# Kernel optimization log

Hardware: AMD Instinct MI355X
Metric: run time of the kernel (lower is better)

Reference implementation:

```python
import jax, jax.numpy as jnp
import numpy as np
import math


def _layernorm(x, g, b, eps=1e-5):
    m = x.mean(-1, keepdims=True)
    v = x.var(-1, keepdims=True)
    return (x - m) / jnp.sqrt(v + eps) * g + b


def _ssd(log_decay, frequency, b_r, b_i, chunk):
    # SSD eigenstate evolution: chunk-local complex decay-mask matmuls + sequential inter-chunk state scan
    B, T, K = b_r.shape
    T_pad = -(-T // chunk) * chunk
    if T_pad > T:
        pad = T_pad - T
        b_r = jnp.pad(b_r, ((0, 0), (0, pad), (0, 0)))
        b_i = jnp.pad(b_i, ((0, 0), (0, pad), (0, 0)))
    n_chunks = T_pad // chunk
    mag = jax.nn.sigmoid(log_decay)                      # (K,)
    pos = jnp.arange(chunk, dtype=b_r.dtype)             # (C,)
    mag_pow = mag[None, :] ** pos[:, None]               # (C,K)
    phases = pos[:, None] * frequency[None, :]           # (C,K)
    kernel_r = mag_pow * jnp.cos(phases)
    kernel_i = mag_pow * jnp.sin(phases)
    diffs = pos[None, :] - pos[:, None]                  # (C,C), faithful to torch: pos.unsqueeze(0)-pos.unsqueeze(1)
    mask = (diffs >= 0).astype(b_r.dtype)[:, :, None]
    idx = jnp.clip(diffs, 0, None).astype(jnp.int32)
    L_r = kernel_r[idx] * mask                           # (C,C,K)
    L_i = kernel_i[idx] * mask
    Br = b_r.reshape(B, n_chunks, chunk, K)
    Bi = b_i.reshape(B, n_chunks, chunk, K)
    # intra-chunk complex contraction
    intra_r = jnp.einsum('ijk,bnjk->bnik', L_r, Br) - jnp.einsum('ijk,bnjk->bnik', L_i, Bi)
    intra_i = jnp.einsum('ijk,bnjk->bnik', L_r, Bi) + jnp.einsum('ijk,bnjk->bnik', L_i, Br)
    prop_r = L_r[:, 0, :]                                # (C,K)
    prop_i = L_i[:, 0, :]

    def step(carry, chunk_in):
        sr, si = carry                                   # (B,K)
        ir, ii = chunk_in                                # (B,C,K)
        corr_r = prop_r[None] * sr[:, None] - prop_i[None] * si[:, None]
        corr_i = prop_r[None] * si[:, None] + prop_i[None] * sr[:, None]
        out_r = ir + corr_r
        out_i = ii + corr_i
        return (out_r[:, -1], out_i[:, -1]), (out_r, out_i)

    init = (jnp.zeros((B, K), b_r.dtype), jnp.zeros((B, K), b_r.dtype))
    _, (o_r, o_i) = jax.lax.scan(step, init, (intra_r.transpose(1, 0, 2, 3), intra_i.transpose(1, 0, 2, 3)))
    c_r = o_r.transpose(1, 0, 2, 3).reshape(B, T_pad, K)[:, :T]
    c_i = o_i.transpose(1, 0, 2, 3).reshape(B, T_pad, K)[:, :T]
    return c_r, c_i


def setup_inputs() -> dict:
    B, T, D, K, H, CONV = 4, 4096, 1024, 64, 4, 4
    Kh = K // H
    mlp = 4 * D
    ks = jax.random.split(jax.random.key(0), 12)

    def n(k, shape, s):
        return (jax.random.normal(k, shape) * s).astype(jnp.float32)

    return {
        'x': n(ks[0], (B, T, D), 1.0),
        'in_proj_w': n(ks[1], (2 * K, D), 1.0 / math.sqrt(D)),
        'conv_w': n(ks[2], (2 * K, 1, CONV), 0.5),
        'conv_b': jnp.zeros((2 * K,), jnp.float32),
        'log_decay': jax.random.uniform(ks[3], (K,), minval=-3.0, maxval=-1.5).astype(jnp.float32),
        'frequency': jnp.linspace(0.0, 2 * math.pi * (1 - 1.0 / K), K).astype(jnp.float32),
        'coupling': (jnp.eye(Kh)[None] + 0.01 * jax.random.normal(ks[4], (H, Kh, Kh)) / math.sqrt(Kh)).astype(jnp.float32),
        'out_proj_w': n(ks[5], (D, 2 * K), 1.0 / math.sqrt(2 * K)),
        'gate_w': n(ks[6], (D, D), 1.0 / math.sqrt(D)),
        'gate_b': jnp.full((D,), -2.0, jnp.float32),
        'mlp_w1': n(ks[7], (mlp, D), 1.0 / math.sqrt(D)),
        'mlp_b1': jnp.zeros((mlp,), jnp.float32),
        'mlp_w2': n(ks[8], (D, mlp), 1.0 / math.sqrt(mlp)),
        'mlp_b2': jnp.zeros((D,), jnp.float32),
        'ln1_g': jnp.ones((D,), jnp.float32), 'ln1_b': jnp.zeros((D,), jnp.float32),
        'ln2_g': jnp.ones((D,), jnp.float32), 'ln2_b': jnp.zeros((D,), jnp.float32),
    }


def reference(x, in_proj_w, conv_w, conv_b, log_decay, frequency, coupling,
              out_proj_w, gate_w, gate_b, mlp_w1, mlp_b1, mlp_w2, mlp_b2,
              ln1_g, ln1_b, ln2_g, ln2_b):
    B, T, D = x.shape
    K2 = in_proj_w.shape[0]
    K = K2 // 2
    CHUNK = 64
    H, Kh = coupling.shape[0], coupling.shape[1]
    residual = x
    xn = _layernorm(x, ln1_g, ln1_b)
    beta = xn @ in_proj_w.T                              # (B,T,2K)
    kconv = conv_w.shape[-1]
    # causal depthwise conv1d (torch pads both sides then truncates to T == left-pad kconv-1)
    bc = jax.lax.conv_general_dilated(
        beta.transpose(0, 2, 1), conv_w, (1,), [(kconv - 1, 0)],
        feature_group_count=K2, dimension_numbers=('NCH', 'OIH', 'NCH'))
    beta = jax.nn.silu((bc + conv_b[None, :, None]).transpose(0, 2, 1))
    beta_r, beta_i = beta[..., :K], beta[..., K:]
    c_r, c_i = _ssd(log_decay, frequency, beta_r, beta_i, CHUNK)
    c_r = jnp.einsum('hjk,bthk->bthj', coupling, c_r.reshape(B, T, H, Kh)).reshape(B, T, K)
    c_i = jnp.einsum('hjk,bthk->bthj', coupling, c_i.reshape(B, T, H, Kh)).reshape(B, T, K)
    eig = jnp.concatenate([c_r, c_i], axis=-1)           # (B,T,2K)
    h = eig @ out_proj_w.T
    gate = jax.nn.sigmoid(xn @ gate_w.T + gate_b)
    x1 = residual + gate * h
    xn2 = _layernorm(x1, ln2_g, ln2_b)
    out = x1 + (jax.nn.silu(xn2 @ mlp_w1.T + mlp_b1) @ mlp_w2.T + mlp_b2)
    return out, eig
```

## Files before the change

kernel.cpp:

```cpp
#include <hip/hip_runtime.h>
#include <hip/hip_bf16.h>


#define FIR_LAG 20

typedef __attribute__((ext_vector_type(8))) short    bf16x8;
typedef __attribute__((ext_vector_type(4))) float    f32x4;
typedef __attribute__((ext_vector_type(4))) unsigned short ushort4_t;

__device__ __forceinline__ unsigned short f2bf(float f) {
    union { __hip_bfloat16 b; unsigned short u; } cv;
    cv.b = __float2bfloat16(f);
    return cv.u;
}
__device__ __forceinline__ float bf2f(unsigned short u) {
    return __uint_as_float((unsigned)u << 16);
}

__device__ __forceinline__ void gload_lds16(const unsigned short* g, unsigned short* l) {
    __builtin_amdgcn_global_load_lds(
        (const __attribute__((address_space(1))) unsigned int*)g,
        (__attribute__((address_space(3))) unsigned int*)l, 16, 0, 0);
}

__global__ __launch_bounds__(256) void cvt5_kernel(
    const float* __restrict__ s0, const float* __restrict__ s1,
    const float* __restrict__ s2, const float* __restrict__ s3,
    const float* __restrict__ s4,
    unsigned short* __restrict__ d0, unsigned short* __restrict__ d1,
    unsigned short* __restrict__ d2, unsigned short* __restrict__ d3,
    unsigned short* __restrict__ d4)
{
    int b = blockIdx.x;
    const float* s; unsigned short* d; int base;
    if      (b < 64)   { s = s0; d = d0; base = b; }
    else if (b < 128)  { s = s1; d = d1; base = b - 64; }
    else if (b < 640)  { s = s2; d = d2; base = b - 128; }
    else if (b < 2688) { s = s3; d = d3; base = b - 640; }
    else               { s = s4; d = d4; base = b - 2688; }
    int i = (base * 256 + threadIdx.x) * 8;
    float4 a = *(const float4*)(s + i);
    float4 c = *(const float4*)(s + i + 4);
    ushort4_t o0 = { f2bf(a.x), f2bf(a.y), f2bf(a.z), f2bf(a.w) };
    ushort4_t o1 = { f2bf(c.x), f2bf(c.y), f2bf(c.z), f2bf(c.w) };
    *(ushort4_t*)(d + i)     = o0;
    *(ushort4_t*)(d + i + 4) = o1;
}

__global__ __launch_bounds__(256) void ln_kernel(
    const float* __restrict__ in, const float* __restrict__ g,
    const float* __restrict__ b, unsigned short* __restrict__ out)
{
    const size_t row = blockIdx.x;
    const int t = threadIdx.x;
    float4 v = ((const float4*)(in + row * 1024))[t];
    float s  = v.x + v.y + v.z + v.w;
    float s2 = v.x*v.x + v.y*v.y + v.z*v.z + v.w*v.w;
    #pragma unroll
    for (int o = 32; o > 0; o >>= 1) {
        s  += __shfl_down(s, o);
        s2 += __shfl_down(s2, o);
    }
    __shared__ float red[8];
    __shared__ float mv[2];
    const int wv = t >> 6;
    if ((t & 63) == 0) { red[wv] = s; red[4 + wv] = s2; }
    __syncthreads();
    if (t == 0) {
        float a  = red[0] + red[1] + red[2] + red[3];
        float a2 = red[4] + red[5] + red[6] + red[7];
        float mean = a * (1.f / 1024.f);
        float var  = a2 * (1.f / 1024.f) - mean * mean;
        mv[0] = mean;
        mv[1] = rsqrtf(var + 1e-5f);
    }
    __syncthreads();
    const float mean = mv[0], rstd = mv[1];
    float4 gg = ((const float4*)g)[t];
    float4 bb = ((const float4*)b)[t];
    ushort4_t o4 = { f2bf((v.x - mean) * rstd * gg.x + bb.x),
                     f2bf((v.y - mean) * rstd * gg.y + bb.y),
                     f2bf((v.z - mean) * rstd * gg.z + bb.z),
                     f2bf((v.w - mean) * rstd * gg.w + bb.w) };
    *(ushort4_t*)(out + row * 1024 + t * 4) = o4;
}

__global__ __launch_bounds__(256) void ln_bf16_kernel(
    const unsigned short* __restrict__ in, const float* __restrict__ g,
    const float* __restrict__ b, unsigned short* __restrict__ out)
{
    const size_t row = blockIdx.x;
    const int t = threadIdx.x;
    ushort4_t u = ((const ushort4_t*)(in + row * 1024))[t];
    float4 v = { bf2f(u.x), bf2f(u.y), bf2f(u.z), bf2f(u.w) };
    float s  = v.x + v.y + v.z + v.w;
    float s2 = v.x*v.x + v.y*v.y + v.z*v.z + v.w*v.w;
    #pragma unroll
    for (int o = 32; o > 0; o >>= 1) {
        s  += __shfl_down(s, o);
        s2 += __shfl_down(s2, o);
    }
    __shared__ float red[8];
    __shared__ float mv[2];
    const int wv = t >> 6;
    if ((t & 63) == 0) { red[wv] = s; red[4 + wv] = s2; }
    __syncthreads();
    if (t == 0) {
        float a  = red[0] + red[1] + red[2] + red[3];
        float a2 = red[4] + red[5] + red[6] + red[7];
        float mean = a * (1.f / 1024.f);
        float var  = a2 * (1.f / 1024.f) - mean * mean;
        mv[0] = mean;
        mv[1] = rsqrtf(var + 1e-5f);
    }
    __syncthreads();
    const float mean = mv[0], rstd = mv[1];
    float4 gg = ((const float4*)g)[t];
    float4 bb = ((const float4*)b)[t];
    ushort4_t o4 = { f2bf((v.x - mean) * rstd * gg.x + bb.x),
                     f2bf((v.y - mean) * rstd * gg.y + bb.y),
                     f2bf((v.z - mean) * rstd * gg.z + bb.z),
                     f2bf((v.w - mean) * rstd * gg.w + bb.w) };
    *(ushort4_t*)(out + row * 1024 + t * 4) = o4;
}

__global__ __launch_bounds__(256) void conv_silu_kernel(
    const float* __restrict__ bp, const float* __restrict__ cw,
    const float* __restrict__ cb, float* __restrict__ beta, int T)
{
    const int idx = blockIdx.x * 256 + threadIdx.x;
    const int c  = idx & 127;
    const int bt = idx >> 7;
    const int t  = bt & (T - 1);
    float acc = cb[c];
    #pragma unroll
    for (int j = 0; j < 4; ++j) {
        int ts = t - 3 + j;
        if (ts >= 0) acc += cw[c * 4 + j] * bp[(size_t)(bt - 3 + j) * 128 + c];
    }
    beta[(size_t)bt * 128 + c] = acc / (1.f + expf(-acc));
}

__global__ __launch_bounds__(256) void fir_coupling_kernel(
    const float* __restrict__ beta, const float* __restrict__ log_decay,
    const float* __restrict__ freq, const float* __restrict__ coup,
    float* __restrict__ eig, unsigned short* __restrict__ eig_bf, int T)
{
    __shared__ float sb[65][128];
    const int blk = blockIdx.x;
    const int nch = T >> 6;
    const int b = blk / nch;
    const int n = blk - b * nch;
    const size_t base = ((size_t)b * T + (size_t)n * 64) * 128;
    const int tid = threadIdx.x;

    #pragma unroll
    for (int it = 0; it < 8; ++it) {
        int f = tid + it * 256;
        int r = f >> 5, c4 = f & 31;
        *(float4*)&sb[1 + r][c4 * 4] =
            *(const float4*)(beta + base + (size_t)r * 128 + c4 * 4);
    }
    if (tid < 32) {
        float4 z = make_float4(0.f, 0.f, 0.f, 0.f);
        *(float4*)&sb[0][tid * 4] =
            (n > 0) ? *(const float4*)(beta + base - 128 + tid * 4) : z;
    }
    __syncthreads();

    const int k  = tid & 63;
    const int tq = tid >> 6;
    const float mag = 1.f / (1.f + expf(-log_decay[k]));
    const float w = freq[k];
    const float rr = mag * cosf(w), ri = mag * sinf(w);
    float cr[16], ci[16];
    #pragma unroll
    for (int m = 0; m < 16; ++m) { cr[m] = 0.f; ci[m] = 0.f; }
    float zr = 1.f, zi = 0.f;
    for (int e = 0; e <= FIR_LAG; ++e) {
        #pragma unroll
        for (int m = 0; m < 16; ++m) {
            int i = tq * 16 + m;
            int src = i + e;
            if (src <= 63) {
                float br = sb[1 + src][k];
                float bi = sb[1 + src][64 + k];
                cr[m] += zr * br - zi * bi;
                ci[m] += zr * bi + zi * br;
            }
        }
        float nzr = zr * rr - zi * ri;
        zi = zr * ri + zi * rr;
        zr = nzr;
    }
    if (tq == 0) {
        cr[0] += sb[0][k];
        ci[0] += sb[0][64 + k];
    }
    __syncthreads();
    #pragma unroll
    for (int m = 0; m < 16; ++m) {
        int i = tq * 16 + m;
        sb[i][k] = cr[m];
        sb[i][64 + k] = ci[m];
    }
    __syncthreads();
    const int h = k >> 4, j = k & 15;
    float cp[16];
    #pragma unroll
    for (int q = 0; q < 16; ++q) cp[q] = coup[(h * 16 + j) * 16 + q];
    #pragma unroll
    for (int m = 0; m < 16; ++m) {
        int i = tq * 16 + m;
        float sr = 0.f, si = 0.f;
        #pragma unroll
        for (int q = 0; q < 16; ++q) {
            sr += cp[q] * sb[i][h * 16 + q];
            si += cp[q] * sb[i][64 + h * 16 + q];
        }
        size_t o = base + (size_t)i * 128;
        eig[o + k]         = sr;
        eig[o + 64 + k]    = si;
        eig_bf[o + k]      = f2bf(sr);
        eig_bf[o + 64 + k] = f2bf(si);
    }
}

__global__ __launch_bounds__(256) void gemm64(
    const unsigned short* __restrict__ A, const unsigned short* __restrict__ B,
    float* __restrict__ C, int M, int N, int K)
{
    constexpr int BK = 32;
    __shared__ unsigned short As[64 * BK];
    __shared__ unsigned short Bs[128 * BK];
    const int tid  = threadIdx.x;
    const int lane = tid & 63;
    const int wn   = tid >> 6;
    const int bm   = blockIdx.x * 64;

    f32x4 acc[4][2];
    #pragma unroll
    for (int m = 0; m < 4; ++m)
        #pragma unroll
        for (int n = 0; n < 2; ++n) acc[m][n] = (f32x4){0.f, 0.f, 0.f, 0.f};

    const int frow = lane & 15;
    const int fk   = (lane >> 4) * 8;
    const int arow = tid >> 2, asc = (tid & 3) * 8;

    for (int k0 = 0; k0 < K; k0 += BK) {
        gload_lds16(A + (size_t)(bm + arow) * K + k0 + asc, As + tid * 8);
        #pragma unroll
        for (int it = 0; it < 2; ++it) {
            int cid = it * 256 + tid;
            int row = cid >> 2, sc = (cid & 3) * 8;
            gload_lds16(B + (size_t)row * K + k0 + sc, Bs + cid * 8);
        }
        __syncthreads();
        bf16x8 af[4], bfr[2];
        #pragma unroll
        for (int m = 0; m < 4; ++m)
            af[m] = *(const bf16x8*)(As + (m * 16 + frow) * BK + fk);
        #pragma unroll
        for (int n = 0; n < 2; ++n)
            bfr[n] = *(const bf16x8*)(Bs + (wn * 32 + n * 16 + frow) * BK + fk);
        #pragma unroll
        for (int m = 0; m < 4; ++m)
            #pragma unroll
            for (int n = 0; n < 2; ++n)
                acc[m][n] = __builtin_amdgcn_mfma_f32_16x16x32_bf16(
                    af[m], bfr[n], acc[m][n], 0, 0, 0);
        __syncthreads();
    }

    const int r0 = (lane >> 4) * 4;
    const int cc = lane & 15;
    #pragma unroll
    for (int m = 0; m < 4; ++m)
        #pragma unroll
        for (int n = 0; n < 2; ++n) {
            const int col = wn * 32 + n * 16 + cc;
            #pragma unroll
            for (int j = 0; j < 4; ++j) {
                const int row = bm + m * 16 + r0 + j;
                C[(size_t)row * N + col] = acc[m][n][j];
            }
        }
}

__global__ __launch_bounds__(256) void gemm128_bf16out(
    const unsigned short* __restrict__ A, const unsigned short* __restrict__ B,
    __hip_bfloat16* __restrict__ C, int M, int N, int K)
{
    constexpr int BM = 128, BN = 128, BK = 32;
    __shared__ unsigned short As[BM * BK];
    __shared__ unsigned short Bs[BN * BK];
    const int tid  = threadIdx.x;
    const int lane = tid & 63;
    const int wave = tid >> 6;
    const int wm = wave >> 1, wn = wave & 1;

    const int nbn = N / BN;
    const int nwg = gridDim.x;
    int orig = blockIdx.x;
    int xcd = orig & 7, ixc = orig >> 3;
    int q = nwg >> 3, r = nwg & 7;
    int wgid = (xcd < r ? xcd * (q + 1) : r * (q + 1) + (xcd - r) * q) + ixc;
    const int bm = (wgid / nbn) * BM;
    const int bn = (wgid % nbn) * BN;

    f32x4 acc[4][4];
    #pragma unroll
    for (int m = 0; m < 4; ++m)
        #pragma unroll
        for (int n = 0; n < 4; ++n) acc[m][n] = (f32x4){0.f, 0.f, 0.f, 0.f};

    const int frow = lane & 15;
    const int fk   = (lane >> 4) * 8;
    const int srow = tid >> 2;
    const int sc   = (tid & 3) * 8;

    for (int k0 = 0; k0 < K; k0 += BK) {
        #pragma unroll
        for (int it = 0; it < 2; ++it) {
            int row = it * 64 + srow;
            int ci  = it * 256 + tid;
            gload_lds16(A + (size_t)(bm + row) * K + k0 + sc, As + ci * 8);
            gload_lds16(B + (size_t)(bn + row) * K + k0 + sc, Bs + ci * 8);
        }
        __syncthreads();
        bf16x8 af[4], bfr[4];
        #pragma unroll
        for (int m = 0; m < 4; ++m)
            af[m] = *(const bf16x8*)(As + (wm * 64 + m * 16 + frow) * BK + fk);
        #pragma unroll
        for (int n = 0; n < 4; ++n)
            bfr[n] = *(const bf16x8*)(Bs + (wn * 64 + n * 16 + frow) * BK + fk);
        #pragma unroll
        for (int m = 0; m < 4; ++m)
            #pragma unroll
            for (int n = 0; n < 4; ++n)
                acc[m][n] = __builtin_amdgcn_mfma_f32_16x16x32_bf16(
                    af[m], bfr[n], acc[m][n], 0, 0, 0);
        __syncthreads();
    }

    const int r0 = (lane >> 4) * 4;
    const int cc = lane & 15;
    #pragma unroll
    for (int m = 0; m < 4; ++m)
        #pragma unroll
        for (int n = 0; n < 4; ++n) {
            const int col = bn + wn * 64 + n * 16 + cc;
            #pragma unroll
            for (int j = 0; j < 4; ++j) {
                const int row = bm + wm * 64 + m * 16 + r0 + j;
                C[(size_t)row * N + col] = __float2bfloat16(acc[m][n][j]);
            }
        }
}

template<int EPI, typename OT>
__global__ __launch_bounds__(512) void gemm256(
    const unsigned short* __restrict__ A, const unsigned short* __restrict__ B,
    OT* __restrict__ C, int M, int N, int K,
    const float* __restrict__ bias,
    const float* __restrict__ p1, const unsigned short* __restrict__ p2)
{
    constexpr int BM = 256, BN = 256, BK = 64;
    __shared__ unsigned short As[2 * 2 * 8192];
    __shared__ unsigned short Bs[2 * 2 * 8192];
    const int tid  = threadIdx.x;
    const int lane = tid & 63;
    const int wave = tid >> 6;
    const int wm = wave >> 2;
    const int wn = wave & 3;

    const int nbn = N / BN;
    const int nwg = gridDim.x;
    int orig = blockIdx.x;
    int xcd = orig & 7, ixc = orig >> 3;
    int q = nwg >> 3, r = nwg & 7;
    int wgid = (xcd < r ? xcd * (q + 1) : r * (q + 1) + (xcd - r) * q) + ixc;
    const int bm = (wgid / nbn) * BM;
    const int bn = (wgid % nbn) * BN;

    f32x4 acc[8][4];
    #pragma unroll
    for (int m = 0; m < 8; ++m)
        #pragma unroll
        for (int n = 0; n < 4; ++n) acc[m][n] = (f32x4){0.f, 0.f, 0.f, 0.f};

    const int frow = lane & 15;
    const int lk   = lane >> 4;

    const unsigned short* Abase = A + (size_t)bm * K;
    const unsigned short* Bbase = B + (size_t)bn * K;

#define STAGE(G, LB, NBUF, KH, K0)                                           \
    {                                                                        \
        _Pragma("unroll")                                                    \
        for (int s = 0; s < 2; ++s) {                                        \
            int cid = s * 512 + tid;                                         \
            int rp  = cid >> 3, cp = cid & 7;                                \
            int c   = cp ^ (rp & 7);                                         \
            int g   = 2 * rp + (c >> 2);                                     \
            gload_lds16((G) + (size_t)g * K + (K0) + (KH) * 32 + (c & 3) * 8,\
                        (LB) + ((NBUF) * 2 + (KH)) * 8192 + cid * 8);        \
        }                                                                    \
    }

#define LDA(MH, KH, BUF)                                                     \
    _Pragma("unroll")                                                        \
    for (int m = 0; m < 4; ++m) {                                            \
        int R  = wm * 128 + (MH) * 64 + m * 16 + frow;                       \
        int rp = R >> 1;                                                     \
        int ch = (((R & 1) << 2) | lk) ^ (rp & 7);                           \
        af[m] = *(const bf16x8*)(As + ((BUF) * 2 + (KH)) * 8192 +            \
                                 rp * 64 + ch * 8);                          \
    }

#define LDB(KH, BUF)                                                         \
    _Pragma("unroll")                                                        \
    for (int n = 0; n < 4; ++n) {                                            \
        int R  = wn * 64 + n * 16 + frow;                                    \
        int rp = R >> 1;                                                     \
        int ch = (((R & 1) << 2) | lk) ^ (rp & 7);                           \
        bfv[n] = *(const bf16x8*)(Bs + ((BUF) * 2 + (KH)) * 8192 +           \
                                  rp * 64 + ch * 8);                         \
    }

#define PH_TAIL(MH)                                                          \
    asm volatile("s_barrier" ::: "memory");                                  \
    asm volatile("s_waitcnt lgkmcnt(0)" ::: "memory");                       \
    __builtin_amdgcn_sched_barrier(0);                                       \
    __builtin_amdgcn_s_setprio(1);                                           \
    _Pragma("unroll")                                                        \
    for (int m = 0; m < 4; ++m)                                              \
        _Pragma("unroll")                                                    \
        for (int n = 0; n < 4; ++n)                                          \
            acc[(MH) * 4 + m][n] = __builtin_amdgcn_mfma_f32_16x16x32_bf16(  \
                af[m], bfv[n], acc[(MH) * 4 + m][n], 0, 0, 0);               \
    __builtin_amdgcn_s_setprio(0);                                           \
    __builtin_amdgcn_sched_barrier(0);

#define VM4 asm volatile("s_waitcnt vmcnt(4)" ::: "memory");
#define VM0 asm volatile("s_waitcnt vmcnt(0)" ::: "memory");

    const int NT = K / BK;

    STAGE(Abase, As, 0, 0, 0)
    STAGE(Bbase, Bs, 0, 0, 0)
    STAGE(Abase, As, 0, 1, 0)
    STAGE(Bbase, Bs, 0, 1, 0)
    VM4
    asm volatile("s_barrier" ::: "memory");

    for (int t = 0; t < NT; ++t) {
        const int buf = t & 1, nbuf = buf ^ 1;
        const int kn = (t + 1) * BK;
        const bool pre = (t + 1 < NT);
        bf16x8 af[4], bfv[4];

        LDA(0, 0, buf)
        LDB(0, buf)
        if (pre) { STAGE(Abase, As, nbuf, 0, kn) }
        PH_TAIL(0)
        LDA(1, 0, buf)
        if (pre) { STAGE(Bbase, Bs, nbuf, 0, kn) VM4 } else { VM0 }
        PH_TAIL(1)
        LDA(0, 1, buf)
        LDB(1, buf)
        if (pre) { STAGE(Abase, As, nbuf, 1, kn) }
        PH_TAIL(0)
        LDA(1, 1, buf)
        if (pre) { STAGE(Bbase, Bs, nbuf, 1, kn) VM4 }
        PH_TAIL(1)
    }
#undef STAGE
#undef LDA
#undef LDB
#undef PH_TAIL
#undef VM4
#undef VM0

    const int r0 = (lane >> 4) * 4;
    const int cc = lane & 15;
    #pragma unroll
    for (int m = 0; m < 8; ++m) {
        #pragma unroll
        for (int n = 0; n < 4; ++n) {
            const int col = bn + wn * 64 + n * 16 + cc;
            #pragma unroll
            for (int j = 0; j < 4; ++j) {
                const int row = bm + wm * 128 + m * 16 + r0 + j;
                const size_t idx = (size_t)row * N + col;
                const float v = acc[m][n][j];
                if constexpr (EPI == 1) {
                    float pre_ = v + bias[col];
                    float gt = 1.f / (1.f + expf(-pre_));
                    C[idx] = (OT)__float2bfloat16(p1[idx] + gt * bf2f(p2[idx]));
                } else if constexpr (EPI == 2) {
                    float pre_ = v + bias[col];
                    C[idx] = (OT)__float2bfloat16(pre_ / (1.f + expf(-pre_)));
                } else {
                    C[idx] = bf2f(p2[idx]) + v + bias[col];
                }
            }
        }
    }
}

extern "C" void kernel_launch(void* const* d_in, const int* in_sizes, int n_in,
                              void* d_out, int out_size, void* d_ws, size_t ws_size,
                              hipStream_t stream)
{
    const float* x        = (const float*)d_in[0];
    const float* in_proj  = (const float*)d_in[1];
    const float* conv_w   = (const float*)d_in[2];
    const float* conv_b   = (const float*)d_in[3];
    const float* log_dec  = (const float*)d_in[4];
    const float* freq     = (const float*)d_in[5];
    const float* coup     = (const float*)d_in[6];
    const float* out_proj = (const float*)d_in[7];
    const float* gate_w   = (const float*)d_in[8];
    const float* gate_b   = (const float*)d_in[9];
    const float* mlp_w1   = (const float*)d_in[10];
    const float* mlp_b1   = (const float*)d_in[11];
    const float* mlp_w2   = (const float*)d_in[12];
    const float* mlp_b2   = (const float*)d_in[13];
    const float* ln1_g    = (const float*)d_in[14];
    const float* ln1_b    = (const float*)d_in[15];
    const float* ln2_g    = (const float*)d_in[16];
    const float* ln2_b    = (const float*)d_in[17];

    const int B = 4, T = 4096, D = 1024;
    const int M = B * T;

    float* out = (float*)d_out;
    float* eig = out + (size_t)M * D;
    float* bpre = eig;

    char* w = (char*)d_ws;
    unsigned short* xn_bf = (unsigned short*)w; w += (size_t)M * 1024 * 2;
    unsigned short* x1_bf = (unsigned short*)w; w += (size_t)M * 1024 * 2;
    float* beta           = (float*)w;          w += (size_t)M * 128 * 4;
    unsigned short* mid   = (unsigned short*)w; w += (size_t)M * 4096 * 2;
    unsigned short* eig_bf= (unsigned short*)w; w += (size_t)M * 128 * 2;
    unsigned short* wb_inproj = (unsigned short*)w; w += (size_t)128 * 1024 * 2;
    unsigned short* wb_outproj= (unsigned short*)w; w += (size_t)1024 * 128 * 2;
    unsigned short* wb_gate   = (unsigned short*)w; w += (size_t)1024 * 1024 * 2;
    unsigned short* wb_mlp1   = (unsigned short*)w; w += (size_t)4096 * 1024 * 2;
    unsigned short* wb_mlp2   = (unsigned short*)w; w += (size_t)1024 * 4096 * 2;
    unsigned short* h_bf = mid;

    cvt5_kernel<<<4736, 256, 0, stream>>>(
        in_proj, out_proj, gate_w, mlp_w1, mlp_w2,
        wb_inproj, wb_outproj, wb_gate, wb_mlp1, wb_mlp2);

    ln_kernel<<<M, 256, 0, stream>>>(x, ln1_g, ln1_b, xn_bf);
    gemm64<<<M / 64, 256, 0, stream>>>(xn_bf, wb_inproj, bpre, M, 128, 1024);
    conv_silu_kernel<<<(M * 128) / 256, 256, 0, stream>>>(bpre, conv_w, conv_b, beta, T);
    fir_coupling_kernel<<<B * (T / 64), 256, 0, stream>>>(
        beta, log_dec, freq, coup, eig, eig_bf, T);
    gemm128_bf16out<<<(M / 128) * (1024 / 128), 256, 0, stream>>>(
        eig_bf, wb_outproj, (__hip_bfloat16*)h_bf, M, 1024, 128);
    gemm256<1, __hip_bfloat16><<<(M / 256) * (1024 / 256), 512, 0, stream>>>(
        xn_bf, wb_gate, (__hip_bfloat16*)x1_bf, M, 1024, 1024, gate_b, x, h_bf);
    ln_bf16_kernel<<<M, 256, 0, stream>>>(x1_bf, ln2_g, ln2_b, xn_bf);
    gemm256<2, __hip_bfloat16><<<(M / 256) * (4096 / 256), 512, 0, stream>>>(
        xn_bf, wb_mlp1, (__hip_bfloat16*)mid, M, 4096, 1024, mlp_b1, nullptr, nullptr);
    gemm256<3, float><<<(M / 256) * (1024 / 256), 512, 0, stream>>>(
        mid, wb_mlp2, out, M, 1024, 4096, mlp_b2, nullptr, x1_bf);
}
```

Before: 519.2 us.

## Fuse conv+SiLU into FIR kernel and add specialized MLP1 GEMM kernel

Folds the causal depthwise conv and SiLU into the FIR/coupling kernel, which now loads the pre-activation tile plus a 4-row halo into shared memory. This removes one launch and the fp32 beta round trip through global memory. Separately, the MLP1 GEMM moves to a new 256x256 kernel with double-buffered LDS, XCD-aware workgroup remapping and a swizzled LDS layout, interleaving prefetch with MFMA phases. The fused kernel uses more shared memory, which may lower occupancy, and it recomputes the halo rows per block.

```diff
diff --git a/kernel.cpp b/kernel.cpp
--- a/kernel.cpp
+++ b/kernel.cpp
@@ -124,47 +124,51 @@
     *(ushort4_t*)(out + row * 1024 + t * 4) = o4;
 }
 
-__global__ __launch_bounds__(256) void conv_silu_kernel(
-    const float* __restrict__ bp, const float* __restrict__ cw,
-    const float* __restrict__ cb, float* __restrict__ beta, int T)
-{
-    const int idx = blockIdx.x * 256 + threadIdx.x;
-    const int c  = idx & 127;
-    const int bt = idx >> 7;
-    const int t  = bt & (T - 1);
-    float acc = cb[c];
-    #pragma unroll
-    for (int j = 0; j < 4; ++j) {
-        int ts = t - 3 + j;
-        if (ts >= 0) acc += cw[c * 4 + j] * bp[(size_t)(bt - 3 + j) * 128 + c];
-    }
-    beta[(size_t)bt * 128 + c] = acc / (1.f + expf(-acc));
-}
-
-__global__ __launch_bounds__(256) void fir_coupling_kernel(
-    const float* __restrict__ beta, const float* __restrict__ log_decay,
+__global__ __launch_bounds__(256) void fir_fused_kernel(
+    const float* __restrict__ bpre, const float* __restrict__ cw,
+    const float* __restrict__ cb, const float* __restrict__ log_decay,
     const float* __restrict__ freq, const float* __restrict__ coup,
     float* __restrict__ eig, unsigned short* __restrict__ eig_bf, int T)
 {
+    __shared__ float sbp[68][128];
     __shared__ float sb[65][128];
     const int blk = blockIdx.x;
     const int nch = T >> 6;
     const int b = blk / nch;
     const int n = blk - b * nch;
-    const size_t base = ((size_t)b * T + (size_t)n * 64) * 128;
+    const int t0 = n * 64;
+    const size_t gbase = ((size_t)b * T + t0) * 128;
     const int tid = threadIdx.x;
 
-    #pragma unroll
-    for (int it = 0; it < 8; ++it) {
-        int f = tid + it * 256;
+    for (int f = tid; f < 68 * 32; f += 256) {
         int r = f >> 5, c4 = f & 31;
-        *(float4*)&sb[1 + r][c4 * 4] =
-            *(const float4*)(beta + base + (size_t)r * 128 + c4 * 4);
-    }
-    if (tid < 32) {
+        int tr = t0 - 4 + r;
         float4 z = make_float4(0.f, 0.f, 0.f, 0.f);
-        *(float4*)&sb[0][tid * 4] =
-            (n > 0) ? *(const float4*)(beta + base - 128 + tid * 4) : z;
+        *(float4*)&sbp[r][c4 * 4] = (tr >= 0)
+            ? *(const float4*)(bpre + ((size_t)b * T + tr) * 128 + c4 * 4)
+            : z;
+    }
+    __syncthreads();
+
+    {
+        const int c = tid & 127;
+        float w0 = cw[c * 4 + 0], w1 = cw[c * 4 + 1];
+        float w2 = cw[c * 4 + 2], w3 = cw[c * 4 + 3];
+        float bc = cb[c];
+        for (int f = tid; f < 65 * 128; f += 256) {
+            int i = f >> 7;
+            int t = t0 - 1 + i;
+            float v = 0.f;
+            if (t >= 0) {
+                float acc = bc;
+                if (t - 3 >= 0) acc += w0 * sbp[i + 0][c];
+                if (t - 2 >= 0) acc += w1 * sbp[i + 1][c];
+                if (t - 1 >= 0) acc += w2 * sbp[i + 2][c];
+                acc += w3 * sbp[i + 3][c];
+                v = acc / (1.f + expf(-acc));
+            }
+            sb[i][c] = v;
+        }
     }
     __syncthreads();
 
@@ -218,7 +222,7 @@
             sr += cp[q] * sb[i][h * 16 + q];
             si += cp[q] * sb[i][64 + h * 16 + q];
         }
-        size_t o = base + (size_t)i * 128;
+        size_t o = gbase + (size_t)i * 128;
         eig[o + k]         = sr;
         eig[o + 64 + k]    = si;
         eig_bf[o + k]      = f2bf(sr);
@@ -500,12 +504,133 @@
                     float pre_ = v + bias[col];
                     float gt = 1.f / (1.f + expf(-pre_));
                     C[idx] = (OT)__float2bfloat16(p1[idx] + gt * bf2f(p2[idx]));
-                } else if constexpr (EPI == 2) {
-                    float pre_ = v + bias[col];
-                    C[idx] = (OT)__float2bfloat16(pre_ / (1.f + expf(-pre_)));
                 } else {
                     C[idx] = bf2f(p2[idx]) + v + bias[col];
                 }
+            }
+        }
+    }
+}
+
+__global__ __launch_bounds__(512) void gemm256h(
+    const unsigned short* __restrict__ A, const unsigned short* __restrict__ B,
+    __hip_bfloat16* __restrict__ C, int M, int N, int K,
+    const float* __restrict__ bias)
+{
+    constexpr int BM = 256, BN = 256, BK = 32;
+    __shared__ unsigned short As[2 * 8192];
+    __shared__ unsigned short Bs[2 * 8192];
+    const int tid  = threadIdx.x;
+    const int lane = tid & 63;
+    const int wave = tid >> 6;
+    const int wm = wave >> 2;
+    const int wn = wave & 3;
+
+    const int nbn = N / BN;
+    const int nwg = gridDim.x;
+    int orig = blockIdx.x;
+    int xcd = orig & 7, ixc = orig >> 3;
+    int q = nwg >> 3, r = nwg & 7;
+    int wgid = (xcd < r ? xcd * (q + 1) : r * (q + 1) + (xcd - r) * q) + ixc;
+    const int bm = (wgid / nbn) * BM;
+    const int bn = (wgid % nbn) * BN;
+
+    f32x4 acc[8][4];
+    #pragma unroll
+    for (int m = 0; m < 8; ++m)
+        #pragma unroll
+        for (int n = 0; n < 4; ++n) acc[m][n] = (f32x4){0.f, 0.f, 0.f, 0.f};
+
+    const int frow = lane & 15;
+    const int lk   = lane >> 4;
+
+    const unsigned short* Abase = A + (size_t)bm * K;
+    const unsigned short* Bbase = B + (size_t)bn * K;
+
+#define STAGEH(G, LB, NBUF, K0)                                              \
+    {                                                                        \
+        _Pragma("unroll")                                                    \
+        for (int s = 0; s < 2; ++s) {                                        \
+            int cid = s * 512 + tid;                                         \
+            int rp  = cid >> 3, cp = cid & 7;                                \
+            int c   = cp ^ (rp & 7);                                         \
+            int g   = 2 * rp + (c >> 2);                                     \
+            gload_lds16((G) + (size_t)g * K + (K0) + (c & 3) * 8,            \
+                        (LB) + (NBUF) * 8192 + cid * 8);                     \
+        }                                                                    \
+    }
+
+#define LDAH(MH, BUF)                                                        \
+    _Pragma("unroll")                                                        \
+    for (int m = 0; m < 4; ++m) {                                            \
+        int R  = wm * 128 + (MH) * 64 + m * 16 + frow;                       \
+        int rp = R >> 1;                                                     \
+        int ch = (((R & 1) << 2) | lk) ^ (rp & 7);                           \
+        af[m] = *(const bf16x8*)(As + (BUF) * 8192 + rp * 64 + ch * 8);      \
+    }
+
+#define LDBH(BUF)                                                            \
+    _Pragma("unroll")                                                        \
+    for (int n = 0; n < 4; ++n) {                                            \
+        int R  = wn * 64 + n * 16 + frow;                                    \
+        int rp = R >> 1;                                                     \
+        int ch = (((R & 1) << 2) | lk) ^ (rp & 7);                           \
+        bfv[n] = *(const bf16x8*)(Bs + (BUF) * 8192 + rp * 64 + ch * 8);     \
+    }
+
+#define PH_TAILH(MH)                                                         \
+    asm volatile("s_barrier" ::: "memory");                                  \
+    asm volatile("s_waitcnt lgkmcnt(0)" ::: "memory");                       \
+    __builtin_amdgcn_sched_barrier(0);                                       \
+    __builtin_amdgcn_s_setprio(1);                                           \
+    _Pragma("unroll")                                                        \
+    for (int m = 0; m < 4; ++m)                                              \
+        _Pragma("unroll")                                                    \
+        for (int n = 0; n < 4; ++n)                                          \
+            acc[(MH) * 4 + m][n] = __builtin_amdgcn_mfma_f32_16x16x32_bf16(  \
+                af[m], bfv[n], acc[(MH) * 4 + m][n], 0, 0, 0);               \
+    __builtin_amdgcn_s_setprio(0);                                           \
+    __builtin_amdgcn_sched_barrier(0);
+
+    const int NT = K / BK;
+
+    STAGEH(Abase, As, 0, 0)
+    STAGEH(Bbase, Bs, 0, 0)
+    asm volatile("s_waitcnt vmcnt(0)" ::: "memory");
+    asm volatile("s_barrier" ::: "memory");
+
+    for (int t = 0; t < NT; ++t) {
+        const int buf = t & 1, nbuf = buf ^ 1;
+        const int kn = (t + 1) * BK;
+        const bool pre = (t + 1 < NT);
+        bf16x8 af[4], bfv[4];
+
+        LDAH(0, buf)
+        LDBH(buf)
+        if (pre) { STAGEH(Abase, As, nbuf, kn) STAGEH(Bbase, Bs, nbuf, kn) }
+        PH_TAILH(0)
+        LDAH(1, buf)
+        asm volatile("s_waitcnt vmcnt(0)" ::: "memory");
+        PH_TAILH(1)
+    }
+#undef STAGEH
+#undef LDAH
+#undef LDBH
+#undef PH_TAILH
+
+    const int r0 = (lane >> 4) * 4;
+    const int cc = lane & 15;
+    #pragma unroll
+    for (int m = 0; m < 8; ++m) {
+        #pragma unroll
+        for (int n = 0; n < 4; ++n) {
+            const int col = bn + wn * 64 + n * 16 + cc;
+            #pragma unroll
+            for (int j = 0; j < 4; ++j) {
+                const int row = bm + wm * 128 + m * 16 + r0 + j;
+                const size_t idx = (size_t)row * N + col;
+                float pre_ = acc[m][n][j] + bias[col];
+                C[idx] = __float2bfloat16(pre_ / (1.f + expf(-pre_)));
             }
         }
     }
@@ -544,7 +669,6 @@
     char* w = (char*)d_ws;
     unsigned short* xn_bf = (unsigned short*)w; w += (size_t)M * 1024 * 2;
     unsigned short* x1_bf = (unsigned short*)w; w += (size_t)M * 1024 * 2;
-    float* beta           = (float*)w;          w += (size_t)M * 128 * 4;
     unsigned short* mid   = (unsigned short*)w; w += (size_t)M * 4096 * 2;
     unsigned short* eig_bf= (unsigned short*)w; w += (size_t)M * 128 * 2;
     unsigned short* wb_inproj = (unsigned short*)w; w += (size_t)128 * 1024 * 2;
@@ -560,16 +684,15 @@
 
     ln_kernel<<<M, 256, 0, stream>>>(x, ln1_g, ln1_b, xn_bf);
     gemm64<<<M / 64, 256, 0, stream>>>(xn_bf, wb_inproj, bpre, M, 128, 1024);
-    conv_silu_kernel<<<(M * 128) / 256, 256, 0, stream>>>(bpre, conv_w, conv_b, beta, T);
-    fir_coupling_kernel<<<B * (T / 64), 256, 0, stream>>>(
-        beta, log_dec, freq, coup, eig, eig_bf, T);
+    fir_fused_kernel<<<B * (T / 64), 256, 0, stream>>>(
+        bpre, conv_w, conv_b, log_dec, freq, coup, eig, eig_bf, T);
     gemm128_bf16out<<<(M / 128) * (1024 / 128), 256, 0, stream>>>(
         eig_bf, wb_outproj, (__hip_bfloat16*)h_bf, M, 1024, 128);
     gemm256<1, __hip_bfloat16><<<(M / 256) * (1024 / 256), 512, 0, stream>>>(
         xn_bf, wb_gate, (__hip_bfloat16*)x1_bf, M, 1024, 1024, gate_b, x, h_bf);
     ln_bf16_kernel<<<M, 256, 0, stream>>>(x1_bf, ln2_g, ln2_b, xn_bf);
-    gemm256<2, __hip_bfloat16><<<(M / 256) * (4096 / 256), 512, 0, stream>>>(
-        xn_bf, wb_mlp1, (__hip_bfloat16*)mid, M, 4096, 1024, mlp_b1, nullptr, nullptr);
+    gemm256h<<<(M / 256) * (4096 / 256), 512, 0, stream>>>(
+        xn_bf, wb_mlp1, (__hip_bfloat16*)mid, M, 4096, 1024, mlp_b1);
     gemm256<3, float><<<(M / 256) * (1024 / 256), 512, 0, stream>>>(
         mid, wb_mlp2, out, M, 1024, 4096, mlp_b2, nullptr, x1_bf);
 }
```

After: 514.7 us. No clear change (-0.9%).
